# Performance work log

Measured on AMD Instinct MI355X. Metric: run time of the kernel, lower is better.

The kernel has to match this reference:

```python
import jax, jax.numpy as jnp
import numpy as np

B, N, D, K = 16, 512, 256, 12  # batch, nodes, node_dim, num edge types (4 arg + 4 arg' + punct +/- + no_edges +/-)
ITERATION_STEPS = 1


def setup_inputs() -> dict:
    key = jax.random.key(0)
    ks = jax.random.split(key, 8)
    node = jax.random.normal(ks[0], (B, N, D), dtype=jnp.float32)
    node_mask = jax.random.randint(ks[1], (B, N), 0, 2, dtype=jnp.int32)
    graphs = jax.random.randint(ks[2], (K, B, N, N), 0, 2, dtype=jnp.int32)
    s = 1.0 / np.sqrt(D)
    Ww = jax.random.normal(ks[3], (1, D), dtype=jnp.float32) * s   # _node_weight_fc
    bw = jnp.zeros((1,), dtype=jnp.float32)
    Ws = jax.random.normal(ks[4], (D, D), dtype=jnp.float32) * s   # _self_node_fc
    bs = jnp.zeros((D,), dtype=jnp.float32)
    Wk = jax.random.normal(ks[5], (K, D, D), dtype=jnp.float32) * s  # 12 bias-free per-edge-type linears
    return {"node": node, "Ww": Ww, "bw": bw, "Ws": Ws, "bs": bs, "Wk": Wk,
            "node_mask": node_mask, "graphs": graphs}


def reference(node, Ww, bw, Ws, bs, Wk, node_mask, graphs):
    dt = node.dtype
    mask = node_mask.astype(dt)
    eye = jnp.eye(N, dtype=dt)
    # dd_graph = mask_row * mask_col * (1 - diag)
    dd = mask[:, None, :] * mask[:, :, None] * (1.0 - eye)          # [B,N,N]
    g = dd[None] * graphs.astype(dt)                                # [K,B,N,N] masked adjacencies
    neigh = g.sum(axis=(0, 3))                                      # [B,N] total neighbor count
    neigh = jnp.where(neigh >= 1, neigh, jnp.ones((), dt))

    all_w = []
    for _ in range(ITERATION_STEPS):
        # (1) node relatedness
        w = jax.nn.sigmoid(node @ Ww.T + bw)[..., 0]                # [B,N]
        all_w.append(w)
        self_info = node @ Ws.T + bs                                # [B,N,D]
        # (2) message propagation for all 12 edge types, batched
        trans = jnp.einsum('bnd,ked->kbne', node, Wk)               # [K,B,N,D] per-type linear (x @ W.T)
        wg = w[None, :, None, :] * g                                # [K,B,N,N] masked node weights
        agg = jnp.einsum('kbmn,kbnd->bmd', wg, trans) / neigh[..., None]
        # (3) update
        node = jax.nn.relu(self_info + agg)

    all_weight = jnp.stack(all_w, axis=1)                           # [B,steps,N]
    return node, all_weight
```

## Files before the change

kernel.cpp:

```cpp
#include <hip/hip_runtime.h>
#include <hip/hip_bf16.h>
#include <math.h>

#define BB 16
#define NN 512
#define DD 256
#define KK 12

typedef __bf16 bf16x8 __attribute__((ext_vector_type(8)));
typedef __bf16 bf16x4 __attribute__((ext_vector_type(4)));
typedef float  f32x4  __attribute__((ext_vector_type(4)));

#define WS_WM     0
#define WS_MASKBF 32768
#define WS_NODEBF 49152
#define WS_NODET  4243456
#define WS_WKBF   8437760
#define WS_WSBF   10010624

__global__ __launch_bounds__(256) void k1_prep(const float* __restrict__ node,
        const float* __restrict__ Ww, const float* __restrict__ bw,
        const int* __restrict__ node_mask,
        float* __restrict__ wm, __bf16* __restrict__ maskbf,
        __bf16* __restrict__ node_bf, float* __restrict__ all_w) {
    int t = threadIdx.x;
    int lane = t & 63;
    int row = blockIdx.x * 4 + (t >> 6);
    const float4 nv = *(const float4*)(node + (size_t)row * DD + lane * 4);
    const float4 wv = *(const float4*)(Ww + lane * 4);
    float dot = nv.x*wv.x + nv.y*wv.y + nv.z*wv.z + nv.w*wv.w;
    #pragma unroll
    for (int off = 32; off > 0; off >>= 1) dot += __shfl_xor(dot, off);
    float w = 1.0f / (1.0f + expf(-(dot + bw[0])));
    int mk = node_mask[row];
    if (lane == 0) {
        wm[row]     = w * (float)mk;
        all_w[row]  = w;
        maskbf[row] = (__bf16)(float)mk;
    }
    bf16x4 nb = {(__bf16)nv.x, (__bf16)nv.y, (__bf16)nv.z, (__bf16)nv.w};
    *(bf16x4*)(node_bf + (size_t)row * DD + lane * 4) = nb;
}

__global__ __launch_bounds__(256) void k1b_convert(const float* __restrict__ Wk,
        const float* __restrict__ Ws, __bf16* __restrict__ Wk_bf, __bf16* __restrict__ Ws_bf) {
    const int KDD = KK * DD * DD;
    int idx = (blockIdx.x * 256 + threadIdx.x) * 4;
    if (idx < KDD) {
        float4 v = *(const float4*)(Wk + idx);
        bf16x4 o = {(__bf16)v.x, (__bf16)v.y, (__bf16)v.z, (__bf16)v.w};
        *(bf16x4*)(Wk_bf + idx) = o;
    } else {
        int j = idx - KDD;
        if (j < DD * DD) {
            float4 v = *(const float4*)(Ws + j);
            bf16x4 o = {(__bf16)v.x, (__bf16)v.y, (__bf16)v.z, (__bf16)v.w};
            *(bf16x4*)(Ws_bf + j) = o;
        }
    }
}

__global__ __launch_bounds__(256) void k2_transpose(const float* __restrict__ node,
        const float* __restrict__ wm, __bf16* __restrict__ dst) {
    __shared__ float tile[64][65];
    int bx = blockIdx.x;
    int b = bx >> 5; int rest = bx & 31; int nt = rest >> 2; int dt = rest & 3;
    int n0 = nt * 64, d0 = dt * 64;
    int t = threadIdx.x;
    #pragma unroll
    for (int i = 0; i < 16; i++) {
        int idx = i * 256 + t;
        int n = idx >> 6, d = idx & 63;
        tile[n][d] = node[((size_t)(b * NN + n0 + n)) * DD + d0 + d];
    }
    __syncthreads();
    #pragma unroll
    for (int i = 0; i < 16; i++) {
        int idx = i * 256 + t;
        int d = idx >> 6, n = idx & 63;
        float w = wm[b * NN + n0 + n];
        dst[((size_t)(b * DD + d0 + d)) * NN + n0 + n] = (__bf16)(tile[n][d] * w);
    }
}

__global__ __launch_bounds__(512, 2) void k45_fused(const int* __restrict__ graphs,
        const int* __restrict__ node_mask, const __bf16* __restrict__ maskbf,
        const __bf16* __restrict__ node_t, const __bf16* __restrict__ node_bf,
        const __bf16* __restrict__ Wk_bf, const __bf16* __restrict__ Ws_bf,
        const float* __restrict__ bs, float* __restrict__ out) {
    __shared__ __align__(16) __bf16 Abf[32][520];
    __shared__ __align__(16) __bf16 Tk[32][264];
    __shared__ float cntp[8][32];
    __shared__ float sm[32];
    int bx = blockIdx.x;
    int b  = (bx & 7) + 8 * ((bx >> 3) & 1);
    int mt = bx >> 4;
    int m0 = mt * 32;
    int t = threadIdx.x;
    int lane = t & 63;
    int w = t >> 6;
    int q = lane >> 4;
    int l16 = lane & 15;
    int esub = w * 32;
    int dsub = w * 32;

    int crow = t >> 7;
    int ccol = (t & 127) * 4;

    f32x4 accO[2][2];
    #pragma unroll
    for (int i = 0; i < 2; i++)
        #pragma unroll
        for (int j = 0; j < 2; j++) accO[i][j] = (f32x4){0.f, 0.f, 0.f, 0.f};
    f32x4 accC[2];
    accC[0] = (f32x4){0.f, 0.f, 0.f, 0.f};
    accC[1] = (f32x4){0.f, 0.f, 0.f, 0.f};

    int4 g[8];
    {
        const int4* gb = (const int4*)(graphs + ((size_t)(b * NN + m0)) * NN);
        #pragma unroll
        for (int u = 0; u < 8; u++) g[u] = gb[u * 512 + t];
    }

    #pragma unroll 1
    for (int k = 0; k < KK; k++) {
        #pragma unroll
        for (int u = 0; u < 8; u++) {
            int row = u * 4 + crow;
            unsigned p0 = (unsigned)g[u].x | ((unsigned)g[u].y << 16);
            unsigned p1 = (unsigned)g[u].z | ((unsigned)g[u].w << 16);
            unsigned drel = (unsigned)(m0 + row - ccol);
            if (drel < 2u)      p0 &= ~(0xFFFFu << (16 * drel));
            else if (drel < 4u) p1 &= ~(0xFFFFu << (16 * (drel - 2)));
            uint2 st; st.x = p0 * 0x3F80u; st.y = p1 * 0x3F80u;
            *(uint2*)&Abf[row][ccol] = st;
        }
        __syncthreads();

        if (k < KK - 1) {
            const int4* gb = (const int4*)(graphs + ((size_t)(((k + 1) * BB + b) * NN + m0)) * NN);
            #pragma unroll
            for (int u = 0; u < 8; u++) g[u] = gb[u * 512 + t];
        }

        f32x4 accT[2][2];
        #pragma unroll
        for (int i = 0; i < 2; i++)
            #pragma unroll
            for (int j = 0; j < 2; j++) accT[i][j] = (f32x4){0.f, 0.f, 0.f, 0.f};
        #pragma unroll
        for (int kk = 0; kk < 16; kk++) {
            int n0c = kk * 32;
            bf16x8 af[2], bfr[2];
            #pragma unroll
            for (int fm = 0; fm < 2; fm++)
                af[fm] = *(const bf16x8*)&Abf[fm * 16 + l16][n0c + q * 8];
            #pragma unroll
            for (int fd = 0; fd < 2; fd++)
                bfr[fd] = *(const bf16x8*)(node_t +
                    ((size_t)(b * DD + esub + fd * 16 + l16)) * NN + n0c + q * 8);
            #pragma unroll
            for (int fm = 0; fm < 2; fm++)
                #pragma unroll
                for (int fd = 0; fd < 2; fd++)
                    accT[fm][fd] = __builtin_amdgcn_mfma_f32_16x16x32_bf16(
                        af[fm], bfr[fd], accT[fm][fd], 0, 0, 0);
            if ((kk >> 1) == w) {
                bf16x8 bfm = (bf16x8){0,0,0,0,0,0,0,0};
                if (l16 == 0)
                    bfm = *(const bf16x8*)(maskbf + b * NN + n0c + q * 8);
                accC[0] = __builtin_amdgcn_mfma_f32_16x16x32_bf16(af[0], bfm, accC[0], 0, 0, 0);
                accC[1] = __builtin_amdgcn_mfma_f32_16x16x32_bf16(af[1], bfm, accC[1], 0, 0, 0);
            }
        }
        #pragma unroll
        for (int fm = 0; fm < 2; fm++)
            #pragma unroll
            for (int fd = 0; fd < 2; fd++) {
                int col = esub + fd * 16 + l16;
                #pragma unroll
                for (int r = 0; r < 4; r++)
                    Tk[fm * 16 + q * 4 + r][col] = (__bf16)accT[fm][fd][r];
            }
        __syncthreads();

        #pragma unroll
        for (int ee = 0; ee < 8; ee++) {
            int e0c = ee * 32;
            bf16x8 afT[2], bw2[2];
            #pragma unroll
            for (int fm = 0; fm < 2; fm++)
                afT[fm] = *(const bf16x8*)&Tk[fm * 16 + l16][e0c + q * 8];
            #pragma unroll
            for (int fd = 0; fd < 2; fd++)
                bw2[fd] = *(const bf16x8*)(Wk_bf +
                    ((size_t)(k * DD + dsub + fd * 16 + l16)) * DD + e0c + q * 8);
            #pragma unroll
            for (int fm = 0; fm < 2; fm++)
                #pragma unroll
                for (int fd = 0; fd < 2; fd++)
                    accO[fm][fd] = __builtin_amdgcn_mfma_f32_16x16x32_bf16(
                        afT[fm], bw2[fd], accO[fm][fd], 0, 0, 0);
        }
    }

    if (l16 == 0) {
        #pragma unroll
        for (int fm = 0; fm < 2; fm++)
            #pragma unroll
            for (int r = 0; r < 4; r++)
                cntp[w][fm * 16 + q * 4 + r] = accC[fm][r];
    }
    __syncthreads();
    if (t < 32) {
        float c = 0.0f;
        #pragma unroll
        for (int w8 = 0; w8 < 8; w8++) c += cntp[w8][t];
        int mk = node_mask[b * NN + m0 + t];
        sm[t] = (float)mk / (c >= 0.5f ? c : 1.0f);
    }
    __syncthreads();

    #pragma unroll
    for (int fm = 0; fm < 2; fm++)
        #pragma unroll
        for (int r = 0; r < 4; r++) {
            float s = sm[fm * 16 + q * 4 + r];
            #pragma unroll
            for (int fd = 0; fd < 2; fd++) accO[fm][fd][r] *= s;
        }

    #pragma unroll
    for (int ee = 0; ee < 8; ee++) {
        int e0c = ee * 32;
        bf16x8 afS[2], bwS[2];
        #pragma unroll
        for (int fm = 0; fm < 2; fm++)
            afS[fm] = *(const bf16x8*)(node_bf +
                ((size_t)(b * NN + m0 + fm * 16 + l16)) * DD + e0c + q * 8);
        #pragma unroll
        for (int fd = 0; fd < 2; fd++)
            bwS[fd] = *(const bf16x8*)(Ws_bf +
                ((size_t)(dsub + fd * 16 + l16)) * DD + e0c + q * 8);
        #pragma unroll
        for (int fm = 0; fm < 2; fm++)
            #pragma unroll
            for (int fd = 0; fd < 2; fd++)
                accO[fm][fd] = __builtin_amdgcn_mfma_f32_16x16x32_bf16(
                    afS[fm], bwS[fd], accO[fm][fd], 0, 0, 0);
    }

    #pragma unroll
    for (int fm = 0; fm < 2; fm++)
        #pragma unroll
        for (int fd = 0; fd < 2; fd++) {
            int d = dsub + fd * 16 + l16;
            float bsv = bs[d];
            #pragma unroll
            for (int r = 0; r < 4; r++) {
                int m = m0 + fm * 16 + q * 4 + r;
                float v = accO[fm][fd][r] + bsv;
                out[((size_t)(b * NN + m)) * DD + d] = fmaxf(v, 0.0f);
            }
        }
}

extern "C" void kernel_launch(void* const* d_in, const int* in_sizes, int n_in,
                              void* d_out, int out_size, void* d_ws, size_t ws_size,
                              hipStream_t stream) {
    const float* node      = (const float*)d_in[0];
    const float* Ww        = (const float*)d_in[1];
    const float* bw        = (const float*)d_in[2];
    const float* Ws        = (const float*)d_in[3];
    const float* bs        = (const float*)d_in[4];
    const float* Wk        = (const float*)d_in[5];
    const int*   node_mask = (const int*)d_in[6];
    const int*   graphs    = (const int*)d_in[7];
    float* out   = (float*)d_out;
    float* all_w = out + (size_t)BB * NN * DD;

    char* ws = (char*)d_ws;
    float*  wm      = (float*)(ws + WS_WM);
    __bf16* maskbf  = (__bf16*)(ws + WS_MASKBF);
    __bf16* node_bf = (__bf16*)(ws + WS_NODEBF);
    __bf16* node_t  = (__bf16*)(ws + WS_NODET);
    __bf16* Wk_bf   = (__bf16*)(ws + WS_WKBF);
    __bf16* Ws_bf   = (__bf16*)(ws + WS_WSBF);

    k1_prep    <<<2048, 256, 0, stream>>>(node, Ww, bw, node_mask, wm, maskbf, node_bf, all_w);
    k1b_convert<<< 832, 256, 0, stream>>>(Wk, Ws, Wk_bf, Ws_bf);
    k2_transpose<<<512, 256, 0, stream>>>(node, wm, node_t);
    k45_fused  <<< 256, 512, 0, stream>>>(graphs, node_mask, maskbf, node_t, node_bf,
                                          Wk_bf, Ws_bf, bs, out);
}
```

Before: 355.0 us.

## Split edge types across two blocks with atomic accumulation and separate epilogue kernel

The fused aggregation kernel now splits the 12 edge types into two halves handled by separate blocks. This doubles the grid from 256 to 512 blocks, so the GPU's compute units stay busier. Partial aggregates and neighbor counts are combined with float atomicAdd into a zero-initialized output and count buffer. A new epilogue kernel then applies normalization, the self-node GEMM, bias and ReLU. The cost is an extra init kernel and an extra epilogue kernel, atomic traffic on the full output, and a re-read of the output.

After: 457.3 us. +28.8%, slower.

```diff
diff --git a/kernel.cpp b/kernel.cpp
--- a/kernel.cpp
+++ b/kernel.cpp
@@ -17,6 +17,19 @@
 #define WS_NODET  4243456
 #define WS_WKBF   8437760
 #define WS_WSBF   10010624
+#define WS_CNT    10141696
+
+__global__ __launch_bounds__(256) void k0_init(float* __restrict__ out, float* __restrict__ cnt) {
+    int idx = blockIdx.x * 256 + threadIdx.x;
+    const int OUT4 = BB * NN * DD / 4;
+    if (idx < OUT4) {
+        *(float4*)(out + (size_t)idx * 4) = (float4){0.f, 0.f, 0.f, 0.f};
+    } else {
+        int j = idx - OUT4;
+        if (j < BB * NN / 4)
+            *(float4*)(cnt + (size_t)j * 4) = (float4){0.f, 0.f, 0.f, 0.f};
+    }
+}
 
 __global__ __launch_bounds__(256) void k1_prep(const float* __restrict__ node,
         const float* __restrict__ Ww, const float* __restrict__ bw,
@@ -83,18 +96,18 @@
     }
 }
 
-__global__ __launch_bounds__(512, 2) void k45_fused(const int* __restrict__ graphs,
-        const int* __restrict__ node_mask, const __bf16* __restrict__ maskbf,
-        const __bf16* __restrict__ node_t, const __bf16* __restrict__ node_bf,
-        const __bf16* __restrict__ Wk_bf, const __bf16* __restrict__ Ws_bf,
-        const float* __restrict__ bs, float* __restrict__ out) {
+__global__ __launch_bounds__(512, 4) void k45_fused(const int* __restrict__ graphs,
+        const __bf16* __restrict__ maskbf,
+        const __bf16* __restrict__ node_t,
+        const __bf16* __restrict__ Wk_bf,
+        float* __restrict__ out, float* __restrict__ cnt) {
     __shared__ __align__(16) __bf16 Abf[32][520];
     __shared__ __align__(16) __bf16 Tk[32][264];
     __shared__ float cntp[8][32];
-    __shared__ float sm[32];
     int bx = blockIdx.x;
     int b  = (bx & 7) + 8 * ((bx >> 3) & 1);
-    int mt = bx >> 4;
+    int kh = (bx >> 4) & 1;
+    int mt = bx >> 5;
     int m0 = mt * 32;
     int t = threadIdx.x;
     int lane = t & 63;
@@ -118,13 +131,14 @@
 
     int4 g[8];
     {
-        const int4* gb = (const int4*)(graphs + ((size_t)(b * NN + m0)) * NN);
+        const int4* gb = (const int4*)(graphs + ((size_t)((kh * 6 * BB + b) * NN + m0)) * NN);
         #pragma unroll
         for (int u = 0; u < 8; u++) g[u] = gb[u * 512 + t];
     }
 
     #pragma unroll 1
-    for (int k = 0; k < KK; k++) {
+    for (int j = 0; j < 6; j++) {
+        int k = kh * 6 + j;
         #pragma unroll
         for (int u = 0; u < 8; u++) {
             int row = u * 4 + crow;
@@ -138,7 +152,7 @@
         }
         __syncthreads();
 
-        if (k < KK - 1) {
+        if (j < 5) {
             const int4* gb = (const int4*)(graphs + ((size_t)(((k + 1) * BB + b) * NN + m0)) * NN);
             #pragma unroll
             for (int u = 0; u < 8; u++) g[u] = gb[u * 512 + t];
@@ -148,7 +162,7 @@
         #pragma unroll
         for (int i = 0; i < 2; i++)
             #pragma unroll
-            for (int j = 0; j < 2; j++) accT[i][j] = (f32x4){0.f, 0.f, 0.f, 0.f};
+            for (int jj = 0; jj < 2; jj++) accT[i][jj] = (f32x4){0.f, 0.f, 0.f, 0.f};
         #pragma unroll
         for (int kk = 0; kk < 16; kk++) {
             int n0c = kk * 32;
@@ -217,20 +231,50 @@
         float c = 0.0f;
         #pragma unroll
         for (int w8 = 0; w8 < 8; w8++) c += cntp[w8][t];
+        atomicAdd(&cnt[b * NN + m0 + t], c);
+    }
+
+    #pragma unroll
+    for (int fm = 0; fm < 2; fm++)
+        #pragma unroll
+        for (int fd = 0; fd < 2; fd++) {
+            int d = dsub + fd * 16 + l16;
+            #pragma unroll
+            for (int r = 0; r < 4; r++) {
+                int m = m0 + fm * 16 + q * 4 + r;
+                atomicAdd(&out[((size_t)(b * NN + m)) * DD + d], accO[fm][fd][r]);
+            }
+        }
+}
+
+__global__ __launch_bounds__(512, 2) void k6_reduce(const int* __restrict__ node_mask,
+        const __bf16* __restrict__ node_bf, const __bf16* __restrict__ Ws_bf,
+        const float* __restrict__ bs, const float* __restrict__ cnt,
+        float* __restrict__ out) {
+    __shared__ float sm[32];
+    int bx = blockIdx.x;
+    int b  = (bx & 7) + 8 * ((bx >> 3) & 1);
+    int mt = bx >> 4;
+    int m0 = mt * 32;
+    int t = threadIdx.x;
+    int lane = t & 63;
+    int w = t >> 6;
+    int q = lane >> 4;
+    int l16 = lane & 15;
+    int dsub = w * 32;
+
+    if (t < 32) {
+        float c = cnt[b * NN + m0 + t];
         int mk = node_mask[b * NN + m0 + t];
         sm[t] = (float)mk / (c >= 0.5f ? c : 1.0f);
     }
     __syncthreads();
 
-    #pragma unroll
-    for (int fm = 0; fm < 2; fm++)
-        #pragma unroll
-        for (int r = 0; r < 4; r++) {
-            float s = sm[fm * 16 + q * 4 + r];
-            #pragma unroll
-            for (int fd = 0; fd < 2; fd++) accO[fm][fd][r] *= s;
-        }
-
+    f32x4 accS[2][2];
+    #pragma unroll
+    for (int i = 0; i < 2; i++)
+        #pragma unroll
+        for (int j = 0; j < 2; j++) accS[i][j] = (f32x4){0.f, 0.f, 0.f, 0.f};
     #pragma unroll
     for (int ee = 0; ee < 8; ee++) {
         int e0c = ee * 32;
@@ -247,8 +291,8 @@
         for (int fm = 0; fm < 2; fm++)
             #pragma unroll
             for (int fd = 0; fd < 2; fd++)
-                accO[fm][fd] = __builtin_amdgcn_mfma_f32_16x16x32_bf16(
-                    afS[fm], bwS[fd], accO[fm][fd], 0, 0, 0);
+                accS[fm][fd] = __builtin_amdgcn_mfma_f32_16x16x32_bf16(
+                    afS[fm], bwS[fd], accS[fm][fd], 0, 0, 0);
     }
 
     #pragma unroll
@@ -260,8 +304,10 @@
             #pragma unroll
             for (int r = 0; r < 4; r++) {
                 int m = m0 + fm * 16 + q * 4 + r;
-                float v = accO[fm][fd][r] + bsv;
-                out[((size_t)(b * NN + m)) * DD + d] = fmaxf(v, 0.0f);
+                size_t idx = ((size_t)(b * NN + m)) * DD + d;
+                float s = sm[fm * 16 + q * 4 + r];
+                float v = s * out[idx] + accS[fm][fd][r] + bsv;
+                out[idx] = fmaxf(v, 0.0f);
             }
         }
 }
@@ -287,10 +333,12 @@
     __bf16* node_t  = (__bf16*)(ws + WS_NODET);
     __bf16* Wk_bf   = (__bf16*)(ws + WS_WKBF);
     __bf16* Ws_bf   = (__bf16*)(ws + WS_WSBF);
-
+    float*  cnt     = (float*)(ws + WS_CNT);
+
+    k0_init    <<<2056, 256, 0, stream>>>(out, cnt);
     k1_prep    <<<2048, 256, 0, stream>>>(node, Ww, bw, node_mask, wm, maskbf, node_bf, all_w);
     k1b_convert<<< 832, 256, 0, stream>>>(Wk, Ws, Wk_bf, Ws_bf);
     k2_transpose<<<512, 256, 0, stream>>>(node, wm, node_t);
-    k45_fused  <<< 256, 512, 0, stream>>>(graphs, node_mask, maskbf, node_t, node_bf,
-                                          Wk_bf, Ws_bf, bs, out);
-}
+    k45_fused  <<< 512, 512, 0, stream>>>(graphs, maskbf, node_t, Wk_bf, out, cnt);
+    k6_reduce  <<< 256, 512, 0, stream>>>(node_mask, node_bf, Ws_bf, bs, cnt, out);
+}
```

## Double-buffer adjacency and T tiles to cut to one barrier per edge type

Applied to the files above, without the earlier changes.

Double-buffers the LDS adjacency tile (Abf) and the intermediate T tile (Tk). The next edge type's adjacency is converted into the spare buffer after the current aggregation MMA loop, and the global load is issued two iterations ahead. This removes one of the two block-wide barriers per edge-type iteration and lets the graph loads overlap more compute. The cost is double the LDS footprint (about 100KB per block), which may threaten the occupancy of two 512-thread blocks per CU. It also uses a custom barrier macro with sched_barrier and lgkmcnt waits.

Result: no change. 348.8 us (-1.7%).

```diff
diff --git a/kernel.cpp b/kernel.cpp
--- a/kernel.cpp
+++ b/kernel.cpp
@@ -17,6 +17,13 @@
 #define WS_NODET  4243456
 #define WS_WKBF   8437760
 #define WS_WSBF   10010624
+
+#define BAR() do { \
+    __builtin_amdgcn_sched_barrier(0); \
+    asm volatile("s_waitcnt lgkmcnt(0)" ::: "memory"); \
+    __builtin_amdgcn_s_barrier(); \
+    __builtin_amdgcn_sched_barrier(0); \
+} while (0)
 
 __global__ __launch_bounds__(256) void k1_prep(const float* __restrict__ node,
         const float* __restrict__ Ww, const float* __restrict__ bw,
@@ -88,8 +95,8 @@
         const __bf16* __restrict__ node_t, const __bf16* __restrict__ node_bf,
         const __bf16* __restrict__ Wk_bf, const __bf16* __restrict__ Ws_bf,
         const float* __restrict__ bs, float* __restrict__ out) {
-    __shared__ __align__(16) __bf16 Abf[32][520];
-    __shared__ __align__(16) __bf16 Tk[32][264];
+    __shared__ __align__(16) __bf16 Abf[2][32][520];
+    __shared__ __align__(16) __bf16 Tk[2][32][264];
     __shared__ float cntp[8][32];
     __shared__ float sm[32];
     int bx = blockIdx.x;
@@ -117,45 +124,48 @@
     accC[1] = (f32x4){0.f, 0.f, 0.f, 0.f};
 
     int4 g[8];
-    {
-        const int4* gb = (const int4*)(graphs + ((size_t)(b * NN + m0)) * NN);
-        #pragma unroll
-        for (int u = 0; u < 8; u++) g[u] = gb[u * 512 + t];
-    }
+
+#define LOADG(kk_) do { \
+        const int4* gb = (const int4*)(graphs + ((size_t)(((kk_) * BB + b) * NN + m0)) * NN); \
+        _Pragma("unroll") \
+        for (int u = 0; u < 8; u++) g[u] = gb[u * 512 + t]; \
+    } while (0)
+
+#define CONVERT(nb_) do { \
+        _Pragma("unroll") \
+        for (int u = 0; u < 8; u++) { \
+            int row = u * 4 + crow; \
+            unsigned p0 = (unsigned)g[u].x | ((unsigned)g[u].y << 16); \
+            unsigned p1 = (unsigned)g[u].z | ((unsigned)g[u].w << 16); \
+            unsigned drel = (unsigned)(m0 + row - ccol); \
+            if (drel < 2u)      p0 &= ~(0xFFFFu << (16 * drel)); \
+            else if (drel < 4u) p1 &= ~(0xFFFFu << (16 * (drel - 2))); \
+            uint2 st; st.x = p0 * 0x3F80u; st.y = p1 * 0x3F80u; \
+            *(uint2*)&Abf[nb_][row][ccol] = st; \
+        } \
+    } while (0)
+
+    LOADG(0);
+    CONVERT(0);
+    LOADG(1);
+    BAR();
+
+    int ac = 0, tc = 0;
 
     #pragma unroll 1
     for (int k = 0; k < KK; k++) {
-        #pragma unroll
-        for (int u = 0; u < 8; u++) {
-            int row = u * 4 + crow;
-            unsigned p0 = (unsigned)g[u].x | ((unsigned)g[u].y << 16);
-            unsigned p1 = (unsigned)g[u].z | ((unsigned)g[u].w << 16);
-            unsigned drel = (unsigned)(m0 + row - ccol);
-            if (drel < 2u)      p0 &= ~(0xFFFFu << (16 * drel));
-            else if (drel < 4u) p1 &= ~(0xFFFFu << (16 * (drel - 2)));
-            uint2 st; st.x = p0 * 0x3F80u; st.y = p1 * 0x3F80u;
-            *(uint2*)&Abf[row][ccol] = st;
-        }
-        __syncthreads();
-
-        if (k < KK - 1) {
-            const int4* gb = (const int4*)(graphs + ((size_t)(((k + 1) * BB + b) * NN + m0)) * NN);
-            #pragma unroll
-            for (int u = 0; u < 8; u++) g[u] = gb[u * 512 + t];
-        }
-
         f32x4 accT[2][2];
         #pragma unroll
         for (int i = 0; i < 2; i++)
             #pragma unroll
-            for (int j = 0; j < 2; j++) accT[i][j] = (f32x4){0.f, 0.f, 0.f, 0.f};
+            for (int jj = 0; jj < 2; jj++) accT[i][jj] = (f32x4){0.f, 0.f, 0.f, 0.f};
         #pragma unroll
         for (int kk = 0; kk < 16; kk++) {
             int n0c = kk * 32;
             bf16x8 af[2], bfr[2];
             #pragma unroll
             for (int fm = 0; fm < 2; fm++)
-                af[fm] = *(const bf16x8*)&Abf[fm * 16 + l16][n0c + q * 8];
+                af[fm] = *(const bf16x8*)&Abf[ac][fm * 16 + l16][n0c + q * 8];
             #pragma unroll
             for (int fd = 0; fd < 2; fd++)
                 bfr[fd] = *(const bf16x8*)(node_t +
@@ -174,6 +184,10 @@
                 accC[1] = __builtin_amdgcn_mfma_f32_16x16x32_bf16(af[1], bfm, accC[1], 0, 0, 0);
             }
         }
+
+        if (k < KK - 1) CONVERT(ac ^ 1);
+        if (k < KK - 2) LOADG(k + 2);
+
         #pragma unroll
         for (int fm = 0; fm < 2; fm++)
             #pragma unroll
@@ -181,9 +195,10 @@
                 int col = esub + fd * 16 + l16;
                 #pragma unroll
                 for (int r = 0; r < 4; r++)
-                    Tk[fm * 16 + q * 4 + r][col] = (__bf16)accT[fm][fd][r];
+                    Tk[tc][fm * 16 + q * 4 + r][col] = (__bf16)accT[fm][fd][r];
             }
-        __syncthreads();
+
+        BAR();
 
         #pragma unroll
         for (int ee = 0; ee < 8; ee++) {
@@ -191,7 +206,7 @@
             bf16x8 afT[2], bw2[2];
             #pragma unroll
             for (int fm = 0; fm < 2; fm++)
-                afT[fm] = *(const bf16x8*)&Tk[fm * 16 + l16][e0c + q * 8];
+                afT[fm] = *(const bf16x8*)&Tk[tc][fm * 16 + l16][e0c + q * 8];
             #pragma unroll
             for (int fd = 0; fd < 2; fd++)
                 bw2[fd] = *(const bf16x8*)(Wk_bf +
@@ -203,6 +218,8 @@
                     accO[fm][fd] = __builtin_amdgcn_mfma_f32_16x16x32_bf16(
                         afT[fm], bw2[fd], accO[fm][fd], 0, 0, 0);
         }
+
+        ac ^= 1; tc ^= 1;
     }
 
     if (l16 == 0) {
@@ -264,6 +281,8 @@
                 out[((size_t)(b * NN + m)) * DD + d] = fmaxf(v, 0.0f);
             }
         }
+#undef LOADG
+#undef CONVERT
 }
 
 extern "C" void kernel_launch(void* const* d_in, const int* in_sizes, int n_in,
```
